# Kernel tuning notes

Hardware: AMD Instinct MI355X
Metric: run time of the kernel (lower is better)

The kernel has to match this reference:

```python
import jax, jax.numpy as jnp
import numpy as np

NX, NY, D, K = 20000, 50000, 64, 8
NUM_BATCHES = 2


def _knn_np(px, py, bx, by, k):
    # Batched exact kNN via chunked squared-distance + argpartition (mirrors torch_cluster.knn under no_grad).
    pp = (px * px).sum(1)
    idx = np.empty((py.shape[0], k), np.int32)
    chunk = 4096
    for s in range(0, py.shape[0], chunk):
        q = py[s:s + chunk]
        d = (q * q).sum(1)[:, None] + pp[None, :] - 2.0 * (q @ px.T)
        d = np.where(by[s:s + chunk, None] == bx[None, :], d, np.inf)
        idx[s:s + chunk] = np.argpartition(d, k, axis=1)[:, :k].astype(np.int32)
    return idx


def setup_inputs() -> dict:
    rng = np.random.default_rng(0)
    pos_x = (rng.random((NX, 3)) * 10.0).astype(np.float32)
    pos_y = (rng.random((NY, 3)) * 10.0).astype(np.float32)
    bx = np.repeat(np.arange(NUM_BATCHES), NX // NUM_BATCHES).astype(np.int32)
    by = np.repeat(np.arange(NUM_BATCHES), NY // NUM_BATCHES).astype(np.int32)
    x_idx = _knn_np(pos_x, pos_y, bx, by, K).reshape(-1)            # [NY*K]
    y_idx = np.repeat(np.arange(NY, dtype=np.int32), K)             # [NY*K]

    key = jax.random.key(0)
    ks = jax.random.split(key, 6)

    def lin(k, fi, fo):
        return jax.random.normal(k, (fi, fo), jnp.float32) / np.sqrt(fi).astype(np.float32)

    return {
        "x": jax.random.normal(ks[0], (NX, D), jnp.float32),
        "pos_x": jnp.asarray(pos_x),
        "pos_y": jnp.asarray(pos_y),
        "x_idx": jnp.asarray(x_idx),
        "y_idx": jnp.asarray(y_idx),
        # ResnetBlockFC 1: size_in=D+3, size_h=D, size_out=D (shortcut linear, no bias)
        "W0a": lin(ks[1], D + 3, D), "b0a": jnp.zeros((D,), jnp.float32),
        "W1a": lin(ks[2], D, D),     "b1a": jnp.zeros((D,), jnp.float32),
        "Wsa": lin(ks[3], D + 3, D),
        # ResnetBlockFC 2: size_in=size_h=size_out=D (identity shortcut)
        "W0b": lin(ks[4], D, D),     "b0b": jnp.zeros((D,), jnp.float32),
        "W1b": lin(ks[5], D, D),     "b1b": jnp.zeros((D,), jnp.float32),
    }


def reference(x, pos_x, pos_y, x_idx, y_idx, W0a, b0a, W1a, b1a, Wsa, W0b, b0b, W1b, b1b):
    # gather + positional diff (diff computed under no_grad in the original)
    diff = jax.lax.stop_gradient(pos_x[x_idx] - pos_y[y_idx])        # [E, 3]
    h = jnp.concatenate([x[x_idx], diff], axis=1)                    # [E, D+3]
    # ResnetBlockFC 1: out = shortcut(h) + fc1(relu(fc0(relu(h))))
    net = jax.nn.relu(h) @ W0a + b0a
    dx = jax.nn.relu(net) @ W1a + b1a
    h = h @ Wsa + dx                                                 # [E, D]
    # ResnetBlockFC 2 (identity shortcut)
    net = jax.nn.relu(h) @ W0b + b0b
    h = h + jax.nn.relu(net) @ W1b + b1b                             # [E, D]
    # scatter-max back to query points (every query has exactly K edges)
    out = jax.ops.segment_max(h, y_idx, num_segments=NY)             # [NY, D]
    return out
```

## Files before the change

### kernel.cpp

```cpp
#include <hip/hip_runtime.h>


typedef _Float16 f16x8 __attribute__((ext_vector_type(8)));
typedef _Float16 f16x4 __attribute__((ext_vector_type(4)));
typedef float    f32x4 __attribute__((ext_vector_type(4)));

constexpr int NX     = 20000;
constexpr int NROWS  = 50000 * 8;
constexpr int NTILES = NROWS / 16;
constexpr int NPAIRS = NTILES / 2;
constexpr int NFRAG  = 48;
constexpr int BW     = 8;
constexpr int BLOCK  = 64 * BW;
constexpr int TS2    = 72;

__global__ void prep_x(const float* __restrict__ x, _Float16* __restrict__ x16) {
    const int i = blockIdx.x * blockDim.x + threadIdx.x;
    if (i < NX * 16) {
        float4 v = ((const float4*)x)[i];
        f16x4 o = {(_Float16)v.x, (_Float16)v.y, (_Float16)v.z, (_Float16)v.w};
        *(f16x4*)(x16 + (size_t)i * 4) = o;
    }
}

static __device__ __forceinline__ void pack_relu(const f32x4* A, f16x8* bf) {
#pragma unroll
    for (int s = 0; s < 2; ++s) {
        f16x8 r;
#pragma unroll
        for (int e = 0; e < 8; ++e) {
            float v = A[2 * s + (e >> 2)][e & 3];
            r[e] = (_Float16)(v > 0.0f ? v : 0.0f);
        }
        bf[s] = r;
    }
}

__global__ __launch_bounds__(BLOCK, 4)
void pointnet_fused(const _Float16* __restrict__ x16,
                    const float* __restrict__ pos_x,
                    const float* __restrict__ pos_y,
                    const int*   __restrict__ x_idx,
                    const float* __restrict__ W0a, const float* __restrict__ b0a,
                    const float* __restrict__ W1a, const float* __restrict__ b1a,
                    const float* __restrict__ Wsa,
                    const float* __restrict__ W0b, const float* __restrict__ b0b,
                    const float* __restrict__ W1b, const float* __restrict__ b1b,
                    float* __restrict__ out)
{
    __shared__ __align__(16) _Float16 bfrag[NFRAG * 64 * 8];
    __shared__ __align__(16) _Float16 ebuf[BW][16 * TS2];
    __shared__ __align__(16) float    bias3f[64];
    __shared__ __align__(16) float    bias5f[64];

    const int tid = threadIdx.x;

    for (int p = tid; p < NFRAG * 64; p += BLOCK) {
        const int f = p >> 6, l = p & 63;
        const int q = l >> 4, n0 = l & 15;
        int grp, fl;
        if      (f < 12) { grp = 0; fl = f; }
        else if (f < 24) { grp = 1; fl = f - 12; }
        else if (f < 32) { grp = 2; fl = f - 24; }
        else if (f < 40) { grp = 3; fl = f - 32; }
        else             { grp = 4; fl = f - 40; }
        const int s = fl >> 2, t = fl & 3;
        const int col = t * 16 + n0;
        f16x8 v;
#pragma unroll
        for (int j = 0; j < 8; ++j) {
            const int k = 32 * s + 8 * q + j;
            float val = 0.0f;
            if      (grp == 0) val = (k < 67) ? W0a[k * 64 + col] : (k == 67 ? b0a[col] : 0.0f);
            else if (grp == 1) val = (k < 67) ? Wsa[k * 64 + col] : (k == 67 ? b1a[col] : 0.0f);
            else {
                const float* W = (grp == 2) ? W1a : (grp == 3) ? W0b : W1b;
                const int row = 32 * s + 16 * (j >> 2) + 4 * q + (j & 3);
                val = W[row * 64 + col];
            }
            v[j] = (_Float16)val;
        }
        *(f16x8*)&bfrag[p * 8] = v;
    }
    if (tid < 64)       bias3f[tid]      = b0b[tid];
    else if (tid < 128) bias5f[tid - 64] = b1b[tid - 64];
    __syncthreads();

    const int lane = tid & 63;
    const int wv   = tid >> 6;
    const int n0   = lane & 15;
    const int q    = lane >> 4;

    _Float16* eb = ebuf[wv];

    const int ey  = (lane >> 3) & 1;
    const int efg = lane & 7;
    const int esb = lane >> 4;

    const int gwave  = blockIdx.x * BW + wv;
    const int nwaves = gridDim.x * BW;

#define WFRAG(fid) (*(const f16x8*)&bfrag[(((fid) * 64) + lane) * 8])

    for (int pr = gwave; pr < NPAIRS; pr += nwaves) {
        const int tA = pr * 2;

        f16x8 h[2][3];
#pragma unroll
        for (int u = 0; u < 2; ++u) {
            const int row = (tA + u) * 16 + n0;
            const int xi  = x_idx[row];
            const _Float16* xp = x16 + (long)xi * 64 + q * 8;
            h[u][0] = *(const f16x8*)(xp);
            h[u][1] = *(const f16x8*)(xp + 32);
            f16x8 z = {};
            h[u][2] = z;
            if (q == 0) {
                const int yi = row >> 3;
#pragma unroll
                for (int j = 0; j < 3; ++j)
                    h[u][2][j] = (_Float16)(pos_x[xi * 3 + j] - pos_y[yi * 3 + j]);
                h[u][2][3] = (_Float16)1.0f;
            }
        }

        f32x4 A2[2][4];
#pragma unroll
        for (int u = 0; u < 2; ++u)
#pragma unroll
            for (int t = 0; t < 4; ++t) A2[u][t] = (f32x4){0.f, 0.f, 0.f, 0.f};
#pragma unroll
        for (int s = 0; s < 3; ++s)
#pragma unroll
            for (int t = 0; t < 4; ++t) {
                const f16x8 w = WFRAG(12 + s * 4 + t);
                A2[0][t] = __builtin_amdgcn_mfma_f32_16x16x32_f16(w, h[0][s], A2[0][t], 0, 0, 0);
                A2[1][t] = __builtin_amdgcn_mfma_f32_16x16x32_f16(w, h[1][s], A2[1][t], 0, 0, 0);
            }

#pragma unroll
        for (int u = 0; u < 2; ++u)
#pragma unroll
            for (int s = 0; s < 3; ++s)
#pragma unroll
                for (int j = 0; j < 8; ++j) {
                    _Float16 v = h[u][s][j];
                    h[u][s][j] = v > (_Float16)0 ? v : (_Float16)0;
                }

        f32x4 A1[2][4];
#pragma unroll
        for (int u = 0; u < 2; ++u)
#pragma unroll
            for (int t = 0; t < 4; ++t) A1[u][t] = (f32x4){0.f, 0.f, 0.f, 0.f};
#pragma unroll
        for (int s = 0; s < 3; ++s)
#pragma unroll
            for (int t = 0; t < 4; ++t) {
                const f16x8 w = WFRAG(s * 4 + t);
                A1[0][t] = __builtin_amdgcn_mfma_f32_16x16x32_f16(w, h[0][s], A1[0][t], 0, 0, 0);
                A1[1][t] = __builtin_amdgcn_mfma_f32_16x16x32_f16(w, h[1][s], A1[1][t], 0, 0, 0);
            }

        f16x8 bf[2][2];
#pragma unroll
        for (int u = 0; u < 2; ++u) pack_relu(A1[u], bf[u]);
#pragma unroll
        for (int s = 0; s < 2; ++s)
#pragma unroll
            for (int t = 0; t < 4; ++t) {
                const f16x8 w = WFRAG(24 + s * 4 + t);
                A2[0][t] = __builtin_amdgcn_mfma_f32_16x16x32_f16(w, bf[0][s], A2[0][t], 0, 0, 0);
                A2[1][t] = __builtin_amdgcn_mfma_f32_16x16x32_f16(w, bf[1][s], A2[1][t], 0, 0, 0);
            }

#pragma unroll
        for (int u = 0; u < 2; ++u) pack_relu(A2[u], bf[u]);
        f32x4 A3[2][4];
#pragma unroll
        for (int u = 0; u < 2; ++u)
#pragma unroll
            for (int t = 0; t < 4; ++t) A3[u][t] = *(const f32x4*)&bias3f[16 * t + 4 * q];
#pragma unroll
        for (int s = 0; s < 2; ++s)
#pragma unroll
            for (int t = 0; t < 4; ++t) {
                const f16x8 w = WFRAG(32 + s * 4 + t);
                A3[0][t] = __builtin_amdgcn_mfma_f32_16x16x32_f16(w, bf[0][s], A3[0][t], 0, 0, 0);
                A3[1][t] = __builtin_amdgcn_mfma_f32_16x16x32_f16(w, bf[1][s], A3[1][t], 0, 0, 0);
            }

#pragma unroll
        for (int u = 0; u < 2; ++u) pack_relu(A3[u], bf[u]);
#pragma unroll
        for (int s = 0; s < 2; ++s)
#pragma unroll
            for (int t = 0; t < 4; ++t) {
                const f16x8 w = WFRAG(40 + s * 4 + t);
                A2[0][t] = __builtin_amdgcn_mfma_f32_16x16x32_f16(w, bf[0][s], A2[0][t], 0, 0, 0);
                A2[1][t] = __builtin_amdgcn_mfma_f32_16x16x32_f16(w, bf[1][s], A2[1][t], 0, 0, 0);
            }

#pragma unroll
        for (int u = 0; u < 2; ++u) {
            const int tile = tA + u;
            __threadfence_block();
#pragma unroll
            for (int t = 0; t < 4; ++t) {
                f16x4 w;
#pragma unroll
                for (int r = 0; r < 4; ++r) w[r] = (_Float16)A2[u][t][r];
                *(f16x4*)&eb[n0 * TS2 + t * 16 + q * 4] = w;
            }
            __threadfence_block();

            const int dr0 = ey * 8 + esb * 2;
            f16x8 ra = *(const f16x8*)&eb[dr0 * TS2 + efg * 8];
            f16x8 rb = *(const f16x8*)&eb[(dr0 + 1) * TS2 + efg * 8];
#pragma unroll
            for (int e = 0; e < 8; ++e) ra[e] = ra[e] > rb[e] ? ra[e] : rb[e];
#pragma unroll
            for (int st = 0; st < 2; ++st) {
                union { f16x8 h; int i[4]; } uu, v2;
                uu.h = ra;
#pragma unroll
                for (int d = 0; d < 4; ++d) v2.i[d] = __shfl_xor(uu.i[d], st == 0 ? 16 : 32, 64);
#pragma unroll
                for (int e = 0; e < 8; ++e) ra[e] = ra[e] > v2.h[e] ? ra[e] : v2.h[e];
            }
            if (esb == 0) {
                const f32x4 bb0 = *(const f32x4*)&bias5f[efg * 8];
                const f32x4 bb1 = *(const f32x4*)&bias5f[efg * 8 + 4];
                float4 f0 = {(float)ra[0] + bb0[0], (float)ra[1] + bb0[1],
                             (float)ra[2] + bb0[2], (float)ra[3] + bb0[3]};
                float4 f1 = {(float)ra[4] + bb1[0], (float)ra[5] + bb1[1],
                             (float)ra[6] + bb1[2], (float)ra[7] + bb1[3]};
                float* op = out + (long)(tile * 2 + ey) * 64 + efg * 8;
                *(float4*)op = f0;
                *(float4*)(op + 4) = f1;
            }
        }
    }
#undef WFRAG
}

extern "C" void kernel_launch(void* const* d_in, const int* in_sizes, int n_in,
                              void* d_out, int out_size, void* d_ws, size_t ws_size,
                              hipStream_t stream) {
    (void)in_sizes; (void)n_in; (void)ws_size; (void)out_size;
    _Float16* x16 = (_Float16*)d_ws;

    prep_x<<<(NX * 16 + 255) / 256, 256, 0, stream>>>((const float*)d_in[0], x16);

    pointnet_fused<<<512, BLOCK, 0, stream>>>(
        x16,
        (const float*)d_in[1],
        (const float*)d_in[2],
        (const int*)  d_in[3],
        (const float*)d_in[5],  (const float*)d_in[6],
        (const float*)d_in[7],  (const float*)d_in[8],
        (const float*)d_in[9],
        (const float*)d_in[10], (const float*)d_in[11],
        (const float*)d_in[12], (const float*)d_in[13],
        (float*)d_out);
}
```

Measured before the change: 123.6 us.

## Precompute per-point first-layer projections and gather them instead of raw features

```diff
diff --git a/kernel.cpp b/kernel.cpp
--- a/kernel.cpp
+++ b/kernel.cpp
@@ -9,18 +9,82 @@
 constexpr int NROWS  = 50000 * 8;
 constexpr int NTILES = NROWS / 16;
 constexpr int NPAIRS = NTILES / 2;
-constexpr int NFRAG  = 48;
+constexpr int NFRAG  = 32;
 constexpr int BW     = 8;
 constexpr int BLOCK  = 64 * BW;
-constexpr int TS2    = 72;
-
-__global__ void prep_x(const float* __restrict__ x, _Float16* __restrict__ x16) {
-    const int i = blockIdx.x * blockDim.x + threadIdx.x;
-    if (i < NX * 16) {
-        float4 v = ((const float4*)x)[i];
-        f16x4 o = {(_Float16)v.x, (_Float16)v.y, (_Float16)v.z, (_Float16)v.w};
-        *(f16x4*)(x16 + (size_t)i * 4) = o;
-    }
+constexpr int NXT    = NX / 16;
+
+#define Z1_OFF  ((size_t)NX * 64)
+#define CTR_OFF ((size_t)NX * 128)
+
+__global__ __launch_bounds__(BLOCK)
+void prep_z(const float* __restrict__ x,
+            const float* __restrict__ W0a, const float* __restrict__ b0a,
+            const float* __restrict__ Wsa, const float* __restrict__ b1a,
+            float* __restrict__ ws)
+{
+    __shared__ __align__(16) _Float16 wfrag[16 * 64 * 8];
+    const int tid = threadIdx.x;
+    for (int p = tid; p < 16 * 64; p += BLOCK) {
+        const int f = p >> 6, l = p & 63;
+        const int q = l >> 4, n0 = l & 15;
+        const int grp = f >> 3, fl = f & 7, s = fl >> 2, t = fl & 3;
+        const int col = t * 16 + n0;
+        const float* W = grp ? Wsa : W0a;
+        f16x8 v;
+#pragma unroll
+        for (int j = 0; j < 8; ++j) {
+            const int k = 32 * s + 8 * q + j;
+            v[j] = (_Float16)W[k * 64 + col];
+        }
+        *(f16x8*)&wfrag[p * 8] = v;
+    }
+    __syncthreads();
+
+    const int lane = tid & 63, wv = tid >> 6;
+    const int n0 = lane & 15, q = lane >> 4;
+    const int tile = blockIdx.x * BW + wv;
+#define PWF(fid) (*(const f16x8*)&wfrag[(((fid) * 64) + lane) * 8])
+    if (tile < NXT) {
+        const float* xr = x + (long)(tile * 16 + n0) * 64 + 8 * q;
+        f16x8 xb[2], xrl[2];
+#pragma unroll
+        for (int s = 0; s < 2; ++s) {
+            f32x4 a = *(const f32x4*)(xr + 32 * s);
+            f32x4 b = *(const f32x4*)(xr + 32 * s + 4);
+#pragma unroll
+            for (int e = 0; e < 4; ++e) {
+                xb[s][e]     = (_Float16)a[e];
+                xb[s][4 + e] = (_Float16)b[e];
+            }
+#pragma unroll
+            for (int e = 0; e < 8; ++e)
+                xrl[s][e] = xb[s][e] > (_Float16)0 ? xb[s][e] : (_Float16)0;
+        }
+        f32x4 AZ[4], AZ1[4];
+#pragma unroll
+        for (int t = 0; t < 4; ++t) {
+            AZ[t]  = *(const f32x4*)(b1a + 16 * t + 4 * q);
+            AZ1[t] = *(const f32x4*)(b0a + 16 * t + 4 * q);
+        }
+#pragma unroll
+        for (int s = 0; s < 2; ++s)
+#pragma unroll
+            for (int t = 0; t < 4; ++t) {
+                AZ[t]  = __builtin_amdgcn_mfma_f32_16x16x32_f16(PWF(8 + s * 4 + t), xb[s],  AZ[t],  0, 0, 0);
+                AZ1[t] = __builtin_amdgcn_mfma_f32_16x16x32_f16(PWF(0 + s * 4 + t), xrl[s], AZ1[t], 0, 0, 0);
+            }
+        float* zr  = ws + (long)(tile * 16 + n0) * 64;
+        float* z1r = ws + Z1_OFF + (long)(tile * 16 + n0) * 64;
+#pragma unroll
+        for (int t = 0; t < 4; ++t) {
+            *(f32x4*)(zr  + 16 * t + 4 * q) = AZ[t];
+            *(f32x4*)(z1r + 16 * t + 4 * q) = AZ1[t];
+        }
+    }
+#undef PWF
+    if (blockIdx.x == 0 && tid == 0)
+        *((unsigned*)(ws + CTR_OFF)) = 0u;
 }
 
 static __device__ __forceinline__ void pack_relu(const f32x4* A, f16x8* bf) {
@@ -37,19 +101,18 @@
 }
 
 __global__ __launch_bounds__(BLOCK, 4)
-void pointnet_fused(const _Float16* __restrict__ x16,
+void pointnet_fused(const float* __restrict__ ws,
                     const float* __restrict__ pos_x,
                     const float* __restrict__ pos_y,
                     const int*   __restrict__ x_idx,
-                    const float* __restrict__ W0a, const float* __restrict__ b0a,
-                    const float* __restrict__ W1a, const float* __restrict__ b1a,
+                    const float* __restrict__ W0a,
+                    const float* __restrict__ W1a,
                     const float* __restrict__ Wsa,
                     const float* __restrict__ W0b, const float* __restrict__ b0b,
                     const float* __restrict__ W1b, const float* __restrict__ b1b,
                     float* __restrict__ out)
 {
     __shared__ __align__(16) _Float16 bfrag[NFRAG * 64 * 8];
-    __shared__ __align__(16) _Float16 ebuf[BW][16 * TS2];
     __shared__ __align__(16) float    bias3f[64];
     __shared__ __align__(16) float    bias5f[64];
 
@@ -58,27 +121,25 @@
     for (int p = tid; p < NFRAG * 64; p += BLOCK) {
         const int f = p >> 6, l = p & 63;
         const int q = l >> 4, n0 = l & 15;
-        int grp, fl;
-        if      (f < 12) { grp = 0; fl = f; }
-        else if (f < 24) { grp = 1; fl = f - 12; }
-        else if (f < 32) { grp = 2; fl = f - 24; }
-        else if (f < 40) { grp = 3; fl = f - 32; }
-        else             { grp = 4; fl = f - 40; }
-        const int s = fl >> 2, t = fl & 3;
-        const int col = t * 16 + n0;
         f16x8 v;
-#pragma unroll
-        for (int j = 0; j < 8; ++j) {
-            const int k = 32 * s + 8 * q + j;
-            float val = 0.0f;
-            if      (grp == 0) val = (k < 67) ? W0a[k * 64 + col] : (k == 67 ? b0a[col] : 0.0f);
-            else if (grp == 1) val = (k < 67) ? Wsa[k * 64 + col] : (k == 67 ? b1a[col] : 0.0f);
-            else {
-                const float* W = (grp == 2) ? W1a : (grp == 3) ? W0b : W1b;
+        if (f < 8) {
+            const int t = f & 3;
+            const int col = t * 16 + n0;
+            const float* W = (f < 4) ? W0a : Wsa;
+#pragma unroll
+            for (int j = 0; j < 8; ++j) {
+                const int k = 64 + 8 * q + j;
+                v[j] = (_Float16)((k < 67) ? W[k * 64 + col] : 0.0f);
+            }
+        } else {
+            const int fl = (f - 8) & 7, s = fl >> 2, t = fl & 3;
+            const int col = t * 16 + n0;
+            const float* W = (f < 16) ? W1a : (f < 24) ? W0b : W1b;
+#pragma unroll
+            for (int j = 0; j < 8; ++j) {
                 const int row = 32 * s + 16 * (j >> 2) + 4 * q + (j & 3);
-                val = W[row * 64 + col];
-            }
-            v[j] = (_Float16)val;
+                v[j] = (_Float16)W[row * 64 + col];
+            }
         }
         *(f16x8*)&bfrag[p * 8] = v;
     }
@@ -91,78 +152,83 @@
     const int n0   = lane & 15;
     const int q    = lane >> 4;
 
-    _Float16* eb = ebuf[wv];
-
-    const int ey  = (lane >> 3) & 1;
-    const int efg = lane & 7;
-    const int esb = lane >> 4;
-
-    const int gwave  = blockIdx.x * BW + wv;
-    const int nwaves = gridDim.x * BW;
+    const float* Zb  = ws;
+    const float* Z1b = ws + Z1_OFF;
+    unsigned* ctr = (unsigned*)(ws + CTR_OFF);
+
+    const unsigned gwave  = blockIdx.x * BW + wv;
+    const unsigned nwaves = gridDim.x * BW;
 
 #define WFRAG(fid) (*(const f16x8*)&bfrag[(((fid) * 64) + lane) * 8])
 
-    for (int pr = gwave; pr < NPAIRS; pr += nwaves) {
-        const int tA = pr * 2;
-
-        f16x8 h[2][3];
+    unsigned pcur = gwave;
+    while (pcur < NPAIRS) {
+        unsigned pnxt = 0;
+        if (lane == 0) pnxt = nwaves + atomicAdd(ctr, 1u);
+
+        const int tA = (int)pcur * 2;
+
+        f32x4 A2[2][4], A1[2][4];
+        f16x8 hd[2], hdr[2];
 #pragma unroll
         for (int u = 0; u < 2; ++u) {
             const int row = (tA + u) * 16 + n0;
             const int xi  = x_idx[row];
-            const _Float16* xp = x16 + (long)xi * 64 + q * 8;
-            h[u][0] = *(const f16x8*)(xp);
-            h[u][1] = *(const f16x8*)(xp + 32);
+            const float* zp  = Zb  + (long)xi * 64 + 4 * q;
+            const float* z1p = Z1b + (long)xi * 64 + 4 * q;
+#pragma unroll
+            for (int t = 0; t < 4; ++t) {
+                A2[u][t] = *(const f32x4*)(zp  + 16 * t);
+                A1[u][t] = *(const f32x4*)(z1p + 16 * t);
+            }
             f16x8 z = {};
-            h[u][2] = z;
+            hd[u] = z;
             if (q == 0) {
                 const int yi = row >> 3;
 #pragma unroll
                 for (int j = 0; j < 3; ++j)
-                    h[u][2][j] = (_Float16)(pos_x[xi * 3 + j] - pos_y[yi * 3 + j]);
-                h[u][2][3] = (_Float16)1.0f;
-            }
-        }
-
-        f32x4 A2[2][4];
+                    hd[u][j] = (_Float16)(pos_x[xi * 3 + j] - pos_y[yi * 3 + j]);
+            }
+#pragma unroll
+            for (int j = 0; j < 8; ++j)
+                hdr[u][j] = hd[u][j] > (_Float16)0 ? hd[u][j] : (_Float16)0;
+        }
+
 #pragma unroll
         for (int u = 0; u < 2; ++u)
 #pragma unroll
-            for (int t = 0; t < 4; ++t) A2[u][t] = (f32x4){0.f, 0.f, 0.f, 0.f};
-#pragma unroll
-        for (int s = 0; s < 3; ++s)
-#pragma unroll
-            for (int t = 0; t < 4; ++t) {
-                const f16x8 w = WFRAG(12 + s * 4 + t);
-                A2[0][t] = __builtin_amdgcn_mfma_f32_16x16x32_f16(w, h[0][s], A2[0][t], 0, 0, 0);
-                A2[1][t] = __builtin_amdgcn_mfma_f32_16x16x32_f16(w, h[1][s], A2[1][t], 0, 0, 0);
-            }
-
+            for (int t = 0; t < 4; ++t) {
+                A2[u][t] = __builtin_amdgcn_mfma_f32_16x16x32_f16(WFRAG(4 + t), hd[u],  A2[u][t], 0, 0, 0);
+                A1[u][t] = __builtin_amdgcn_mfma_f32_16x16x32_f16(WFRAG(0 + t), hdr[u], A1[u][t], 0, 0, 0);
+            }
+
+        f16x8 bf[2][2];
+#pragma unroll
+        for (int u = 0; u < 2; ++u) pack_relu(A1[u], bf[u]);
+#pragma unroll
+        for (int s = 0; s < 2; ++s)
+#pragma unroll
+            for (int t = 0; t < 4; ++t) {
+                const f16x8 w = WFRAG(8 + s * 4 + t);
+                A2[0][t] = __builtin_amdgcn_mfma_f32_16x16x32_f16(w, bf[0][s], A2[0][t], 0, 0, 0);
+                A2[1][t] = __builtin_amdgcn_mfma_f32_16x16x32_f16(w, bf[1][s], A2[1][t], 0, 0, 0);
+            }
+
+#pragma unroll
+        for (int u = 0; u < 2; ++u) pack_relu(A2[u], bf[u]);
 #pragma unroll
         for (int u = 0; u < 2; ++u)
 #pragma unroll
-            for (int s = 0; s < 3; ++s)
-#pragma unroll
-                for (int j = 0; j < 8; ++j) {
-                    _Float16 v = h[u][s][j];
-                    h[u][s][j] = v > (_Float16)0 ? v : (_Float16)0;
-                }
-
-        f32x4 A1[2][4];
-#pragma unroll
-        for (int u = 0; u < 2; ++u)
-#pragma unroll
-            for (int t = 0; t < 4; ++t) A1[u][t] = (f32x4){0.f, 0.f, 0.f, 0.f};
-#pragma unroll
-        for (int s = 0; s < 3; ++s)
-#pragma unroll
-            for (int t = 0; t < 4; ++t) {
-                const f16x8 w = WFRAG(s * 4 + t);
-                A1[0][t] = __builtin_amdgcn_mfma_f32_16x16x32_f16(w, h[0][s], A1[0][t], 0, 0, 0);
-                A1[1][t] = __builtin_amdgcn_mfma_f32_16x16x32_f16(w, h[1][s], A1[1][t], 0, 0, 0);
-            }
-
-        f16x8 bf[2][2];
+            for (int t = 0; t < 4; ++t) A1[u][t] = *(const f32x4*)&bias3f[16 * t + 4 * q];
+#pragma unroll
+        for (int s = 0; s < 2; ++s)
+#pragma unroll
+            for (int t = 0; t < 4; ++t) {
+                const f16x8 w = WFRAG(16 + s * 4 + t);
+                A1[0][t] = __builtin_amdgcn_mfma_f32_16x16x32_f16(w, bf[0][s], A1[0][t], 0, 0, 0);
+                A1[1][t] = __builtin_amdgcn_mfma_f32_16x16x32_f16(w, bf[1][s], A1[1][t], 0, 0, 0);
+            }
+
 #pragma unroll
         for (int u = 0; u < 2; ++u) pack_relu(A1[u], bf[u]);
 #pragma unroll
@@ -175,71 +241,48 @@
             }
 
 #pragma unroll
-        for (int u = 0; u < 2; ++u) pack_relu(A2[u], bf[u]);
-        f32x4 A3[2][4];
-#pragma unroll
-        for (int u = 0; u < 2; ++u)
-#pragma unroll
-            for (int t = 0; t < 4; ++t) A3[u][t] = *(const f32x4*)&bias3f[16 * t + 4 * q];
-#pragma unroll
-        for (int s = 0; s < 2; ++s)
-#pragma unroll
-            for (int t = 0; t < 4; ++t) {
-                const f16x8 w = WFRAG(32 + s * 4 + t);
-                A3[0][t] = __builtin_amdgcn_mfma_f32_16x16x32_f16(w, bf[0][s], A3[0][t], 0, 0, 0);
-                A3[1][t] = __builtin_amdgcn_mfma_f32_16x16x32_f16(w, bf[1][s], A3[1][t], 0, 0, 0);
-            }
-
-#pragma unroll
-        for (int u = 0; u < 2; ++u) pack_relu(A3[u], bf[u]);
-#pragma unroll
-        for (int s = 0; s < 2; ++s)
-#pragma unroll
-            for (int t = 0; t < 4; ++t) {
-                const f16x8 w = WFRAG(40 + s * 4 + t);
-                A2[0][t] = __builtin_amdgcn_mfma_f32_16x16x32_f16(w, bf[0][s], A2[0][t], 0, 0, 0);
-                A2[1][t] = __builtin_amdgcn_mfma_f32_16x16x32_f16(w, bf[1][s], A2[1][t], 0, 0, 0);
-            }
-
-#pragma unroll
         for (int u = 0; u < 2; ++u) {
-            const int tile = tA + u;
-            __threadfence_block();
-#pragma unroll
-            for (int t = 0; t < 4; ++t) {
-                f16x4 w;
-#pragma unroll
-                for (int r = 0; r < 4; ++r) w[r] = (_Float16)A2[u][t][r];
-                *(f16x4*)&eb[n0 * TS2 + t * 16 + q * 4] = w;
-            }
-            __threadfence_block();
-
-            const int dr0 = ey * 8 + esb * 2;
-            f16x8 ra = *(const f16x8*)&eb[dr0 * TS2 + efg * 8];
-            f16x8 rb = *(const f16x8*)&eb[(dr0 + 1) * TS2 + efg * 8];
-#pragma unroll
-            for (int e = 0; e < 8; ++e) ra[e] = ra[e] > rb[e] ? ra[e] : rb[e];
-#pragma unroll
-            for (int st = 0; st < 2; ++st) {
-                union { f16x8 h; int i[4]; } uu, v2;
-                uu.h = ra;
-#pragma unroll
-                for (int d = 0; d < 4; ++d) v2.i[d] = __shfl_xor(uu.i[d], st == 0 ? 16 : 32, 64);
-#pragma unroll
-                for (int e = 0; e < 8; ++e) ra[e] = ra[e] > v2.h[e] ? ra[e] : v2.h[e];
-            }
-            if (esb == 0) {
-                const f32x4 bb0 = *(const f32x4*)&bias5f[efg * 8];
-                const f32x4 bb1 = *(const f32x4*)&bias5f[efg * 8 + 4];
-                float4 f0 = {(float)ra[0] + bb0[0], (float)ra[1] + bb0[1],
-                             (float)ra[2] + bb0[2], (float)ra[3] + bb0[3]};
-                float4 f1 = {(float)ra[4] + bb1[0], (float)ra[5] + bb1[1],
-                             (float)ra[6] + bb1[2], (float)ra[7] + bb1[3]};
-                float* op = out + (long)(tile * 2 + ey) * 64 + efg * 8;
-                *(float4*)op = f0;
-                *(float4*)(op + 4) = f1;
-            }
-        }
+            union U { f16x8 h; int i[4]; };
+            U pa, pb;
+#pragma unroll
+            for (int e = 0; e < 8; ++e) {
+                pa.h[e] = (_Float16)A2[u][(e >> 2)][e & 3];
+                pb.h[e] = (_Float16)A2[u][2 + (e >> 2)][e & 3];
+            }
+#pragma unroll
+            for (int st = 0; st < 3; ++st) {
+                const int m = 1 << st;
+                U qa, qb;
+#pragma unroll
+                for (int d = 0; d < 4; ++d) {
+                    qa.i[d] = __shfl_xor(pa.i[d], m, 64);
+                    qb.i[d] = __shfl_xor(pb.i[d], m, 64);
+                }
+#pragma unroll
+                for (int e = 0; e < 8; ++e) {
+                    pa.h[e] = pa.h[e] > qa.h[e] ? pa.h[e] : qa.h[e];
+                    pb.h[e] = pb.h[e] > qb.h[e] ? pb.h[e] : qb.h[e];
+                }
+            }
+            if ((n0 & 7) == 0) {
+                const int y = (tA + u) * 2 + (n0 >> 3);
+                float* op = out + (long)y * 64;
+#pragma unroll
+                for (int t = 0; t < 4; ++t) {
+                    const f32x4 bb = *(const f32x4*)&bias5f[16 * t + 4 * q];
+                    const int e0 = (t & 1) * 4;
+                    float4 vst;
+                    if (t < 2) vst = {(float)pa.h[e0 + 0] + bb[0], (float)pa.h[e0 + 1] + bb[1],
+                                      (float)pa.h[e0 + 2] + bb[2], (float)pa.h[e0 + 3] + bb[3]};
+                    else       vst = {(float)pb.h[e0 + 0] + bb[0], (float)pb.h[e0 + 1] + bb[1],
+                                      (float)pb.h[e0 + 2] + bb[2], (float)pb.h[e0 + 3] + bb[3]};
+                    *(float4*)(op + 16 * t + 4 * q) = vst;
+                }
+            }
+        }
+
+        pnxt = (unsigned)__shfl((int)pnxt, 0);
+        pcur = pnxt;
     }
 #undef WFRAG
 }
@@ -248,17 +291,21 @@
                               void* d_out, int out_size, void* d_ws, size_t ws_size,
                               hipStream_t stream) {
     (void)in_sizes; (void)n_in; (void)ws_size; (void)out_size;
-    _Float16* x16 = (_Float16*)d_ws;
-
-    prep_x<<<(NX * 16 + 255) / 256, 256, 0, stream>>>((const float*)d_in[0], x16);
+    float* ws = (float*)d_ws;
+
+    prep_z<<<(NXT + BW - 1) / BW, BLOCK, 0, stream>>>(
+        (const float*)d_in[0],
+        (const float*)d_in[5], (const float*)d_in[6],
+        (const float*)d_in[9], (const float*)d_in[8],
+        ws);
 
     pointnet_fused<<<512, BLOCK, 0, stream>>>(
-        x16,
+        ws,
         (const float*)d_in[1],
         (const float*)d_in[2],
         (const int*)  d_in[3],
-        (const float*)d_in[5],  (const float*)d_in[6],
-        (const float*)d_in[7],  (const float*)d_in[8],
+        (const float*)d_in[5],
+        (const float*)d_in[7],
         (const float*)d_in[9],
         (const float*)d_in[10], (const float*)d_in[11],
         (const float*)d_in[12], (const float*)d_in[13],
```

After: 277.3 us. +124.4%, slower.

## Use atomic work-stealing scheduler, shuffle-based segment max, and higher occupancy

Applied to the files above, without the earlier changes.

```diff
diff --git a/kernel.cpp b/kernel.cpp
--- a/kernel.cpp
+++ b/kernel.cpp
@@ -12,15 +12,20 @@
 constexpr int NFRAG  = 48;
 constexpr int BW     = 8;
 constexpr int BLOCK  = 64 * BW;
-constexpr int TS2    = 72;
-
-__global__ void prep_x(const float* __restrict__ x, _Float16* __restrict__ x16) {
+constexpr int GRID   = 768;
+
+#define CTR_BYTE_OFF ((size_t)NX * 64 * 2)
+
+__global__ void prep_x(const float* __restrict__ x, char* __restrict__ ws) {
+    _Float16* x16 = (_Float16*)ws;
     const int i = blockIdx.x * blockDim.x + threadIdx.x;
     if (i < NX * 16) {
         float4 v = ((const float4*)x)[i];
         f16x4 o = {(_Float16)v.x, (_Float16)v.y, (_Float16)v.z, (_Float16)v.w};
         *(f16x4*)(x16 + (size_t)i * 4) = o;
     }
+    if (blockIdx.x == 0 && threadIdx.x == 0)
+        *(unsigned*)(ws + CTR_BYTE_OFF) = 0u;
 }
 
 static __device__ __forceinline__ void pack_relu(const f32x4* A, f16x8* bf) {
@@ -36,8 +41,8 @@
     }
 }
 
-__global__ __launch_bounds__(BLOCK, 4)
-void pointnet_fused(const _Float16* __restrict__ x16,
+__global__ __launch_bounds__(BLOCK, 6)
+void pointnet_fused(char* __restrict__ ws,
                     const float* __restrict__ pos_x,
                     const float* __restrict__ pos_y,
                     const int*   __restrict__ x_idx,
@@ -49,9 +54,11 @@
                     float* __restrict__ out)
 {
     __shared__ __align__(16) _Float16 bfrag[NFRAG * 64 * 8];
-    __shared__ __align__(16) _Float16 ebuf[BW][16 * TS2];
     __shared__ __align__(16) float    bias3f[64];
     __shared__ __align__(16) float    bias5f[64];
+
+    const _Float16* x16 = (const _Float16*)ws;
+    unsigned* ctr = (unsigned*)(ws + CTR_BYTE_OFF);
 
     const int tid = threadIdx.x;
 
@@ -91,19 +98,17 @@
     const int n0   = lane & 15;
     const int q    = lane >> 4;
 
-    _Float16* eb = ebuf[wv];
-
-    const int ey  = (lane >> 3) & 1;
-    const int efg = lane & 7;
-    const int esb = lane >> 4;
-
-    const int gwave  = blockIdx.x * BW + wv;
-    const int nwaves = gridDim.x * BW;
+    const unsigned gwave  = blockIdx.x * BW + wv;
+    const unsigned nwaves = GRID * BW;
 
 #define WFRAG(fid) (*(const f16x8*)&bfrag[(((fid) * 64) + lane) * 8])
 
-    for (int pr = gwave; pr < NPAIRS; pr += nwaves) {
-        const int tA = pr * 2;
+    unsigned pcur = gwave;
+    while (pcur < NPAIRS) {
+        unsigned pnxt = 0;
+        if (lane == 0) pnxt = nwaves + atomicAdd(ctr, 1u);
+
+        const int tA = (int)pcur * 2;
 
         f16x8 h[2][3];
 #pragma unroll
@@ -176,22 +181,21 @@
 
 #pragma unroll
         for (int u = 0; u < 2; ++u) pack_relu(A2[u], bf[u]);
-        f32x4 A3[2][4];
-#pragma unroll
-        for (int u = 0; u < 2; ++u)
-#pragma unroll
-            for (int t = 0; t < 4; ++t) A3[u][t] = *(const f32x4*)&bias3f[16 * t + 4 * q];
+#pragma unroll
+        for (int u = 0; u < 2; ++u)
+#pragma unroll
+            for (int t = 0; t < 4; ++t) A1[u][t] = *(const f32x4*)&bias3f[16 * t + 4 * q];
 #pragma unroll
         for (int s = 0; s < 2; ++s)
 #pragma unroll
             for (int t = 0; t < 4; ++t) {
                 const f16x8 w = WFRAG(32 + s * 4 + t);
-                A3[0][t] = __builtin_amdgcn_mfma_f32_16x16x32_f16(w, bf[0][s], A3[0][t], 0, 0, 0);
-                A3[1][t] = __builtin_amdgcn_mfma_f32_16x16x32_f16(w, bf[1][s], A3[1][t], 0, 0, 0);
-            }
-
-#pragma unroll
-        for (int u = 0; u < 2; ++u) pack_relu(A3[u], bf[u]);
+                A1[0][t] = __builtin_amdgcn_mfma_f32_16x16x32_f16(w, bf[0][s], A1[0][t], 0, 0, 0);
+                A1[1][t] = __builtin_amdgcn_mfma_f32_16x16x32_f16(w, bf[1][s], A1[1][t], 0, 0, 0);
+            }
+
+#pragma unroll
+        for (int u = 0; u < 2; ++u) pack_relu(A1[u], bf[u]);
 #pragma unroll
         for (int s = 0; s < 2; ++s)
 #pragma unroll
@@ -203,43 +207,47 @@
 
 #pragma unroll
         for (int u = 0; u < 2; ++u) {
-            const int tile = tA + u;
-            __threadfence_block();
-#pragma unroll
-            for (int t = 0; t < 4; ++t) {
-                f16x4 w;
-#pragma unroll
-                for (int r = 0; r < 4; ++r) w[r] = (_Float16)A2[u][t][r];
-                *(f16x4*)&eb[n0 * TS2 + t * 16 + q * 4] = w;
-            }
-            __threadfence_block();
-
-            const int dr0 = ey * 8 + esb * 2;
-            f16x8 ra = *(const f16x8*)&eb[dr0 * TS2 + efg * 8];
-            f16x8 rb = *(const f16x8*)&eb[(dr0 + 1) * TS2 + efg * 8];
-#pragma unroll
-            for (int e = 0; e < 8; ++e) ra[e] = ra[e] > rb[e] ? ra[e] : rb[e];
-#pragma unroll
-            for (int st = 0; st < 2; ++st) {
-                union { f16x8 h; int i[4]; } uu, v2;
-                uu.h = ra;
-#pragma unroll
-                for (int d = 0; d < 4; ++d) v2.i[d] = __shfl_xor(uu.i[d], st == 0 ? 16 : 32, 64);
-#pragma unroll
-                for (int e = 0; e < 8; ++e) ra[e] = ra[e] > v2.h[e] ? ra[e] : v2.h[e];
-            }
-            if (esb == 0) {
-                const f32x4 bb0 = *(const f32x4*)&bias5f[efg * 8];
-                const f32x4 bb1 = *(const f32x4*)&bias5f[efg * 8 + 4];
-                float4 f0 = {(float)ra[0] + bb0[0], (float)ra[1] + bb0[1],
-                             (float)ra[2] + bb0[2], (float)ra[3] + bb0[3]};
-                float4 f1 = {(float)ra[4] + bb1[0], (float)ra[5] + bb1[1],
-                             (float)ra[6] + bb1[2], (float)ra[7] + bb1[3]};
-                float* op = out + (long)(tile * 2 + ey) * 64 + efg * 8;
-                *(float4*)op = f0;
-                *(float4*)(op + 4) = f1;
-            }
-        }
+            union U { f16x8 h; int i[4]; };
+            U pa, pb;
+#pragma unroll
+            for (int e = 0; e < 8; ++e) {
+                pa.h[e] = (_Float16)A2[u][(e >> 2)][e & 3];
+                pb.h[e] = (_Float16)A2[u][2 + (e >> 2)][e & 3];
+            }
+#pragma unroll
+            for (int st = 0; st < 3; ++st) {
+                const int m = 1 << st;
+                U qa, qb;
+#pragma unroll
+                for (int d = 0; d < 4; ++d) {
+                    qa.i[d] = __shfl_xor(pa.i[d], m, 64);
+                    qb.i[d] = __shfl_xor(pb.i[d], m, 64);
+                }
+#pragma unroll
+                for (int e = 0; e < 8; ++e) {
+                    pa.h[e] = pa.h[e] > qa.h[e] ? pa.h[e] : qa.h[e];
+                    pb.h[e] = pb.h[e] > qb.h[e] ? pb.h[e] : qb.h[e];
+                }
+            }
+            if ((n0 & 7) == 0) {
+                const int y = (tA + u) * 2 + (n0 >> 3);
+                float* op = out + (long)y * 64;
+#pragma unroll
+                for (int t = 0; t < 4; ++t) {
+                    const f32x4 bb = *(const f32x4*)&bias5f[16 * t + 4 * q];
+                    const int e0 = (t & 1) * 4;
+                    float4 vst;
+                    if (t < 2) vst = {(float)pa.h[e0 + 0] + bb[0], (float)pa.h[e0 + 1] + bb[1],
+                                      (float)pa.h[e0 + 2] + bb[2], (float)pa.h[e0 + 3] + bb[3]};
+                    else       vst = {(float)pb.h[e0 + 0] + bb[0], (float)pb.h[e0 + 1] + bb[1],
+                                      (float)pb.h[e0 + 2] + bb[2], (float)pb.h[e0 + 3] + bb[3]};
+                    *(float4*)(op + 16 * t + 4 * q) = vst;
+                }
+            }
+        }
+
+        pnxt = (unsigned)__shfl((int)pnxt, 0);
+        pcur = pnxt;
     }
 #undef WFRAG
 }
@@ -248,12 +256,12 @@
                               void* d_out, int out_size, void* d_ws, size_t ws_size,
                               hipStream_t stream) {
     (void)in_sizes; (void)n_in; (void)ws_size; (void)out_size;
-    _Float16* x16 = (_Float16*)d_ws;
-
-    prep_x<<<(NX * 16 + 255) / 256, 256, 0, stream>>>((const float*)d_in[0], x16);
-
-    pointnet_fused<<<512, BLOCK, 0, stream>>>(
-        x16,
+    char* ws = (char*)d_ws;
+
+    prep_x<<<(NX * 16 + 255) / 256, 256, 0, stream>>>((const float*)d_in[0], ws);
+
+    pointnet_fused<<<GRID, BLOCK, 0, stream>>>(
+        ws,
         (const float*)d_in[1],
         (const float*)d_in[2],
         (const int*)  d_in[3],
```

Result: slower. 460.5 us (+272.7%).

## Replace static grid-stride tile loop with atomic-counter dynamic work stealing

Applied to the files above, without the earlier changes.

```diff
diff --git a/kernel.cpp b/kernel.cpp
--- a/kernel.cpp
+++ b/kernel.cpp
@@ -12,15 +12,21 @@
 constexpr int NFRAG  = 48;
 constexpr int BW     = 8;
 constexpr int BLOCK  = 64 * BW;
+constexpr int GRID   = 512;
 constexpr int TS2    = 72;
 
-__global__ void prep_x(const float* __restrict__ x, _Float16* __restrict__ x16) {
+#define CTR_BYTE_OFF ((size_t)NX * 64 * 2)
+
+__global__ void prep_x(const float* __restrict__ x, char* __restrict__ ws) {
+    _Float16* x16 = (_Float16*)ws;
     const int i = blockIdx.x * blockDim.x + threadIdx.x;
     if (i < NX * 16) {
         float4 v = ((const float4*)x)[i];
         f16x4 o = {(_Float16)v.x, (_Float16)v.y, (_Float16)v.z, (_Float16)v.w};
         *(f16x4*)(x16 + (size_t)i * 4) = o;
     }
+    if (blockIdx.x == 0 && threadIdx.x == 0)
+        *(unsigned*)(ws + CTR_BYTE_OFF) = 0u;
 }
 
 static __device__ __forceinline__ void pack_relu(const f32x4* A, f16x8* bf) {
@@ -37,7 +43,7 @@
 }
 
 __global__ __launch_bounds__(BLOCK, 4)
-void pointnet_fused(const _Float16* __restrict__ x16,
+void pointnet_fused(char* __restrict__ ws,
                     const float* __restrict__ pos_x,
                     const float* __restrict__ pos_y,
                     const int*   __restrict__ x_idx,
@@ -53,6 +59,9 @@
     __shared__ __align__(16) float    bias3f[64];
     __shared__ __align__(16) float    bias5f[64];
 
+    const _Float16* x16 = (const _Float16*)ws;
+    unsigned* ctr = (unsigned*)(ws + CTR_BYTE_OFF);
+
     const int tid = threadIdx.x;
 
     for (int p = tid; p < NFRAG * 64; p += BLOCK) {
@@ -97,13 +106,17 @@
     const int efg = lane & 7;
     const int esb = lane >> 4;
 
-    const int gwave  = blockIdx.x * BW + wv;
-    const int nwaves = gridDim.x * BW;
+    const unsigned gwave  = blockIdx.x * BW + wv;
+    const unsigned nwaves = GRID * BW;
 
 #define WFRAG(fid) (*(const f16x8*)&bfrag[(((fid) * 64) + lane) * 8])
 
-    for (int pr = gwave; pr < NPAIRS; pr += nwaves) {
-        const int tA = pr * 2;
+    unsigned pcur = gwave;
+    while (pcur < NPAIRS) {
+        unsigned pnxt = 0;
+        if (lane == 0) pnxt = nwaves + atomicAdd(ctr, 1u);
+
+        const int tA = (int)pcur * 2;
 
         f16x8 h[2][3];
 #pragma unroll
@@ -176,22 +189,21 @@
 
 #pragma unroll
         for (int u = 0; u < 2; ++u) pack_relu(A2[u], bf[u]);
-        f32x4 A3[2][4];
-#pragma unroll
-        for (int u = 0; u < 2; ++u)
-#pragma unroll
-            for (int t = 0; t < 4; ++t) A3[u][t] = *(const f32x4*)&bias3f[16 * t + 4 * q];
+#pragma unroll
+        for (int u = 0; u < 2; ++u)
+#pragma unroll
+            for (int t = 0; t < 4; ++t) A1[u][t] = *(const f32x4*)&bias3f[16 * t + 4 * q];
 #pragma unroll
         for (int s = 0; s < 2; ++s)
 #pragma unroll
             for (int t = 0; t < 4; ++t) {
                 const f16x8 w = WFRAG(32 + s * 4 + t);
-                A3[0][t] = __builtin_amdgcn_mfma_f32_16x16x32_f16(w, bf[0][s], A3[0][t], 0, 0, 0);
-                A3[1][t] = __builtin_amdgcn_mfma_f32_16x16x32_f16(w, bf[1][s], A3[1][t], 0, 0, 0);
-            }
-
-#pragma unroll
-        for (int u = 0; u < 2; ++u) pack_relu(A3[u], bf[u]);
+                A1[0][t] = __builtin_amdgcn_mfma_f32_16x16x32_f16(w, bf[0][s], A1[0][t], 0, 0, 0);
+                A1[1][t] = __builtin_amdgcn_mfma_f32_16x16x32_f16(w, bf[1][s], A1[1][t], 0, 0, 0);
+            }
+
+#pragma unroll
+        for (int u = 0; u < 2; ++u) pack_relu(A1[u], bf[u]);
 #pragma unroll
         for (int s = 0; s < 2; ++s)
 #pragma unroll
@@ -240,6 +252,9 @@
                 *(float4*)(op + 4) = f1;
             }
         }
+
+        pnxt = (unsigned)__shfl((int)pnxt, 0);
+        pcur = pnxt;
     }
 #undef WFRAG
 }
@@ -248,12 +263,12 @@
                               void* d_out, int out_size, void* d_ws, size_t ws_size,
                               hipStream_t stream) {
     (void)in_sizes; (void)n_in; (void)ws_size; (void)out_size;
-    _Float16* x16 = (_Float16*)d_ws;
-
-    prep_x<<<(NX * 16 + 255) / 256, 256, 0, stream>>>((const float*)d_in[0], x16);
-
-    pointnet_fused<<<512, BLOCK, 0, stream>>>(
-        x16,
+    char* ws = (char*)d_ws;
+
+    prep_x<<<(NX * 16 + 255) / 256, 256, 0, stream>>>((const float*)d_in[0], ws);
+
+    pointnet_fused<<<GRID, BLOCK, 0, stream>>>(
+        ws,
         (const float*)d_in[1],
         (const float*)d_in[2],
         (const int*)  d_in[3],
```

Result: slower. 249.1 us (+101.6%).
